# Optimization experiments

Hardware: AMD Instinct MI355X
Metric: run time of the kernel (lower is better)

Reference implementation:

```python
import math
import jax, jax.numpy as jnp
import numpy as np

B, T = 65536, 34
VOCAB, TOK_DIM, POS_DIM, D_MODEL, FFN_DIM, HEAD_DIM = 14, 2, 3, 5, 2, 5
EPS = 1e-5

def _pos_flat_idx():
    # replicate _build_pos_map: 10 digits, Z_HI, 10 digits, Z_HI, 10 digits, special0, special1
    sources, indices = [], []
    for _ in range(3):
        for i in range(10):
            sources.append(0); indices.append(i)
        sources.append(2); indices.append(len([s for s in sources if s == 2]) - 1)
    # fix: the torch code appends (2,0),(2,1) after first two digit blocks and (1,0),(2,2) after the third
    sources, indices = [], []
    for i in range(10): sources.append(0); indices.append(i)
    sources.append(2); indices.append(0)
    for i in range(10): sources.append(0); indices.append(i)
    sources.append(2); indices.append(1)
    for i in range(10): sources.append(0); indices.append(i)
    sources.append(1); indices.append(0)
    sources.append(2); indices.append(2)
    src = np.array(sources); idx = np.array(indices)
    # table layout: rows 0..9 digit_pos, row 10 z_hi_pos, rows 11..13 special (learned0, learned1, eos)
    offs = np.array([0, 10, 11])
    return offs[src] + idx  # (34,)

POS_FLAT = jnp.asarray(_pos_flat_idx())
CAUSAL = jnp.tril(jnp.ones((T, T), dtype=bool))

def _rms(x, w):
    return x * jax.lax.rsqrt(jnp.mean(x * x, -1, keepdims=True) + EPS) * w

def setup_inputs():
    key = jax.random.key(0)
    ks = jax.random.split(key, 16)
    n = lambda i, shape: jax.random.normal(ks[i], shape, jnp.float32) * 0.5
    return {
        'idx': jax.random.randint(ks[0], (B, T), 0, VOCAB),
        'tok_emb': n(1, (VOCAB, TOK_DIM)),
        'spiral_amp': jnp.float32(1.0),
        'spiral_phase': jnp.float32(0.1),
        'spiral_slope': jnp.float32(1.0 / 9.0),
        'spiral_offset': jnp.float32(0.05),
        'pos_corr_slope': jnp.float32(0.01),
        'pos_corr_intercept': jnp.float32(0.02),
        'z_hi_pos': n(2, (1, POS_DIM)),
        'special_pos': n(3, (2, POS_DIM)),
        'q_w': n(4, (HEAD_DIM, POS_DIM)),
        'v_w': n(5, (HEAD_DIM, TOK_DIM)),
        'out_A': n(6, (HEAD_DIM, 2)),
        'out_B': n(7, (2, D_MODEL)),
        'q_phase': n(8, (1,)),
        'ln1_w': jnp.ones((D_MODEL,), jnp.float32),
        'ln2_w': jnp.ones((D_MODEL,), jnp.float32),
        'lnf_w': jnp.ones((D_MODEL,), jnp.float32),
        'fc1_w': n(9, (FFN_DIM, D_MODEL)),
        'fc1_b': n(10, (FFN_DIM,)),
        'fc2_w': n(11, (D_MODEL, FFN_DIM)),
        'fc2_b': n(12, (D_MODEL,)),
        'head_w': n(13, (TOK_DIM, D_MODEL)),
    }

def reference(idx, tok_emb, spiral_amp, spiral_phase, spiral_slope, spiral_offset,
              pos_corr_slope, pos_corr_intercept, z_hi_pos, special_pos,
              q_w, v_w, out_A, out_B, q_phase, ln1_w, ln2_w, lnf_w,
              fc1_w, fc1_b, fc2_w, fc2_b, head_w):
    # learned spiral digit positions (10, 3)
    i = jnp.arange(10, dtype=jnp.float32)
    angle = 2.0 * math.pi * i / 10.0 + spiral_phase
    base = jnp.stack([spiral_amp * jnp.cos(angle),
                      spiral_amp * jnp.sin(angle),
                      spiral_slope * i + spiral_offset], -1)
    corr = pos_corr_intercept + pos_corr_slope * i
    digit_pos = base * (1.0 + corr)[:, None]
    table = jnp.concatenate([digit_pos, z_hi_pos, special_pos,
                             jnp.zeros((1, POS_DIM), jnp.float32)], 0)  # (14, 3)
    pos = table[POS_FLAT]  # (T, 3)

    tok = tok_emb[idx]  # (B, T, 2)
    x = jnp.concatenate([tok, jnp.broadcast_to(pos, (idx.shape[0], T, POS_DIM))], -1)  # (B,T,5)

    h = _rms(x, ln1_w)
    q = jnp.einsum('btp,dp->btd', h[..., TOK_DIM:], q_w)  # (B,T,5)
    k = q  # q_proj applied to same input for both q and k
    v = jnp.einsum('btp,dp->btd', h[..., :TOK_DIM], v_w)  # (B,T,5)

    # per-head 2D rotation on first 4 dims (HEAD_DIM//2 = 2 pairs), dim 4 unchanged
    c, s = jnp.cos(q_phase[0]), jnp.sin(q_phase[0])
    q0, q1 = q[..., 0:4:2], q[..., 1:4:2]
    q_rot = jnp.concatenate([
        jnp.stack([q0 * c - q1 * s, q0 * s + q1 * c], -1).reshape(q.shape[:-1] + (4,)),
        q[..., 4:]], -1)

    att = jnp.einsum('btd,bsd->bts', q_rot, k) / math.sqrt(HEAD_DIM)
    att = jnp.where(CAUSAL, att, -jnp.inf)
    att = jax.nn.softmax(att, -1)
    out = jnp.einsum('bts,bsd->btd', att, v)  # (B,T,5)

    x = x + (out @ out_A) @ out_B  # low-rank out_proj
    hh = _rms(x, ln2_w)
    x = x + (jax.nn.gelu(hh @ fc1_w.T + fc1_b, approximate=False) @ fc2_w.T + fc2_b)
    x = _rms(x, lnf_w)
    return (x @ head_w.T) @ tok_emb.T  # (B, T, 14)
```

## Files before the change

kernel.cpp:

```cpp
#include <hip/hip_runtime.h>
#include <math.h>

#define T_SEQ 34
#define NTOK 14
#define NE (T_SEQ * NTOK)
#define ROWS 15
#define BLK 512
#define NEL (ROWS * T_SEQ)
#define TTS 17

__global__ __launch_bounds__(BLK) void micro_fused_kernel(
    const int* __restrict__ idx,
    const float* __restrict__ tok_emb,
    const float* __restrict__ s_amp, const float* __restrict__ s_phase,
    const float* __restrict__ s_slope, const float* __restrict__ s_offset,
    const float* __restrict__ pc_slope, const float* __restrict__ pc_int,
    const float* __restrict__ z_hi, const float* __restrict__ spec,
    const float* __restrict__ q_w, const float* __restrict__ v_w,
    const float* __restrict__ out_A, const float* __restrict__ out_B,
    const float* __restrict__ q_phase,
    const float* __restrict__ ln1_w, const float* __restrict__ ln2_w,
    const float* __restrict__ lnf_w,
    const float* __restrict__ fc1_w, const float* __restrict__ fc1_b,
    const float* __restrict__ fc2_w, const float* __restrict__ fc2_b,
    const float* __restrict__ head_w,
    float* __restrict__ out, int N)
{
    __shared__ float4 H4[NE];
    __shared__ float  H1f[NE];
    __shared__ float4 C3[NE];
    __shared__ int    toksT[T_SEQ * TTS];
    alignas(16) __shared__ float PosT[T_SEQ * 3];
    alignas(16) __shared__ float TE[NTOK * 2];
    alignas(16) __shared__ float PMs[12];
    alignas(16) __shared__ float WsT[NTOK * 8];
    alignas(16) __shared__ float ln2s[8], lnfs[8], fc1ws[12], fc2ws[12], fc2bs[8];
    __shared__ float fc1bs[2];

    const int tid = threadIdx.x;
    const int elemBase = blockIdx.x * NEL;

    if (tid < NEL) {
        int g = elemBase + tid;
        int v = (g < N) ? idx[g] : 0;
        int r = tid / T_SEQ, s = tid - r * T_SEQ;
        toksT[s * TTS + r] = v;
    }

    if (tid < NE) {
        const float amp = s_amp[0], ph = s_phase[0], slp = s_slope[0], off = s_offset[0];
        const float pcs = pc_slope[0], pci = pc_int[0];
        const float cph = cosf(q_phase[0]), sph = sinf(q_phase[0]);
        const float cscale = 0.44721359549995793f * 1.4426950408889634f;
        const int e = tid;
        const int t = e / NTOK, tk = e - t * NTOK;
        float px, py, pz;
        if (t == 33)      { px = 0.f;     py = 0.f;     pz = 0.f; }
        else if (t == 32) { px = z_hi[0]; py = z_hi[1]; pz = z_hi[2]; }
        else if (t == 10) { px = spec[0]; py = spec[1]; pz = spec[2]; }
        else if (t == 21) { px = spec[3]; py = spec[4]; pz = spec[5]; }
        else {
            int i = (t < 10) ? t : (t < 21 ? t - 11 : t - 22);
            float fi = (float)i;
            float ang = 0.62831853071795864769f * fi + ph;
            float mlt = 1.f + pci + pcs * fi;
            px = amp * cosf(ang) * mlt;
            py = amp * sinf(ang) * mlt;
            pz = (slp * fi + off) * mlt;
        }
        if (tk == 0) { PosT[t*3] = px; PosT[t*3+1] = py; PosT[t*3+2] = pz; }
        float x0 = tok_emb[tk * 2], x1 = tok_emb[tk * 2 + 1];
        float ssum = x0*x0 + x1*x1 + px*px + py*py + pz*pz;
        float rn = rsqrtf(ssum * 0.2f + 1e-5f);
        float h0 = x0 * rn * ln1_w[0], h1 = x1 * rn * ln1_w[1];
        float h2 = px * rn * ln1_w[2], h3 = py * rn * ln1_w[3], h4 = pz * rn * ln1_w[4];
        float q0 = q_w[0]  * h2 + q_w[1]  * h3 + q_w[2]  * h4;
        float q1 = q_w[3]  * h2 + q_w[4]  * h3 + q_w[5]  * h4;
        float q2 = q_w[6]  * h2 + q_w[7]  * h3 + q_w[8]  * h4;
        float q3 = q_w[9]  * h2 + q_w[10] * h3 + q_w[11] * h4;
        float q4 = q_w[12] * h2 + q_w[13] * h3 + q_w[14] * h4;
        float r0 = q0 * cph - q1 * sph, r1 = q0 * sph + q1 * cph;
        float r2c = q2 * cph - q3 * sph, r3 = q2 * sph + q3 * cph;
        float c0 = (r0*q_w[0] + r1*q_w[3] + r2c*q_w[6] + r3*q_w[9]  + q4*q_w[12]) * cscale;
        float c1 = (r0*q_w[1] + r1*q_w[4] + r2c*q_w[7] + r3*q_w[10] + q4*q_w[13]) * cscale;
        float c2 = (r0*q_w[2] + r1*q_w[5] + r2c*q_w[8] + r3*q_w[11] + q4*q_w[14]) * cscale;
        H4[e] = make_float4(h2, h3, h4, h0);
        H1f[e] = h1;
        C3[e] = make_float4(c0, c1, c2, 0.f);
    }
    if (tid < 28) TE[tid] = tok_emb[tid];
    if (tid < 70) {
        int v = tid / 5, d = tid - v * 5;
        WsT[v * 8 + d] = head_w[d] * tok_emb[v * 2] + head_w[5 + d] * tok_emb[v * 2 + 1];
    }
    if (tid < 10) {
        int j = tid >> 1, c = tid & 1;
        float acc = 0.f;
        for (int i = 0; i < 5; ++i) {
            float m5 = out_A[i*2] * out_B[j] + out_A[i*2+1] * out_B[5 + j];
            acc += m5 * v_w[i*2 + c];
        }
        PMs[tid] = acc;
    }
    if (tid < 5)  { ln2s[tid] = ln2_w[tid]; lnfs[tid] = lnf_w[tid]; fc2bs[tid] = fc2_b[tid]; }
    if (tid < 10) { fc1ws[tid] = fc1_w[tid]; fc2ws[tid] = fc2_w[tid]; }
    if (tid < 2)  { fc1bs[tid] = fc1_b[tid]; }

    __syncthreads();

    if (tid >= NEL) return;
    const int t = tid / ROWS;
    const int r = tid - t * ROWS;
    const int lin = elemBase + r * T_SEQ + t;

    const int tokt = toksT[t * TTS + r];
    const float4 c3 = C3[t * NTOK + tokt];
    float l = 0.f, a0 = 0.f, a1 = 0.f;
#pragma unroll 4
    for (int s = 0; s <= t; ++s) {
        int tok = toksT[s * TTS + r];
        int e = s * NTOK + tok;
        float4 h = H4[e];
        float h1v = H1f[e];
        float sc = fmaf(c3.x, h.x, fmaf(c3.y, h.y, c3.z * h.z));
        float p = __builtin_amdgcn_exp2f(sc);
        l += p;
        a0 = fmaf(p, h.w, a0);
        a1 = fmaf(p, h1v, a1);
    }
    const float il = __builtin_amdgcn_rcpf(l);
    a0 *= il; a1 *= il;

    if (lin >= N) return;

    const float xv0 = TE[tokt * 2], xv1 = TE[tokt * 2 + 1];
    const float xv2 = PosT[t*3], xv3 = PosT[t*3+1], xv4 = PosT[t*3+2];

    float y[5];
    y[0] = xv0 + PMs[0] * a0 + PMs[1] * a1;
    y[1] = xv1 + PMs[2] * a0 + PMs[3] * a1;
    y[2] = xv2 + PMs[4] * a0 + PMs[5] * a1;
    y[3] = xv3 + PMs[6] * a0 + PMs[7] * a1;
    y[4] = xv4 + PMs[8] * a0 + PMs[9] * a1;

    float s2 = y[0]*y[0] + y[1]*y[1] + y[2]*y[2] + y[3]*y[3] + y[4]*y[4];
    float r2 = rsqrtf(s2 * 0.2f + 1e-5f);
    float hh[5];
#pragma unroll
    for (int j = 0; j < 5; ++j) hh[j] = y[j] * r2 * ln2s[j];

    float u0 = fc1bs[0], u1 = fc1bs[1];
#pragma unroll
    for (int j = 0; j < 5; ++j) { u0 += hh[j] * fc1ws[j]; u1 += hh[j] * fc1ws[5 + j]; }
    float g0 = 0.5f * u0 * (1.f + erff(u0 * 0.70710678118654752f));
    float g1v = 0.5f * u1 * (1.f + erff(u1 * 0.70710678118654752f));

    float y2[5]; float s3 = 0.f;
#pragma unroll
    for (int j = 0; j < 5; ++j) {
        y2[j] = y[j] + g0 * fc2ws[j * 2] + g1v * fc2ws[j * 2 + 1] + fc2bs[j];
        s3 += y2[j] * y2[j];
    }
    float r3 = rsqrtf(s3 * 0.2f + 1e-5f);
    float z[5];
#pragma unroll
    for (int j = 0; j < 5; ++j) z[j] = y2[j] * r3 * lnfs[j];

    float2* op = (float2*)(out + (size_t)lin * 14);
#pragma unroll
    for (int v = 0; v < 7; ++v) {
        float4 w0 = *(const float4*)&WsT[(2*v) * 8];
        float  w4 = WsT[(2*v) * 8 + 4];
        float4 u0v = *(const float4*)&WsT[(2*v+1) * 8];
        float  u4 = WsT[(2*v+1) * 8 + 4];
        float rA = z[0]*w0.x + z[1]*w0.y + z[2]*w0.z + z[3]*w0.w + z[4]*w4;
        float rB = z[0]*u0v.x + z[1]*u0v.y + z[2]*u0v.z + z[3]*u0v.w + z[4]*u4;
        op[v] = make_float2(rA, rB);
    }
}

extern "C" void kernel_launch(void* const* d_in, const int* in_sizes, int n_in,
                              void* d_out, int out_size, void* d_ws, size_t ws_size,
                              hipStream_t stream) {
    const int N = in_sizes[0];
    const int grid = (N + NEL - 1) / NEL;
    micro_fused_kernel<<<grid, BLK, 0, stream>>>(
        (const int*)d_in[0],
        (const float*)d_in[1], (const float*)d_in[2], (const float*)d_in[3],
        (const float*)d_in[4], (const float*)d_in[5], (const float*)d_in[6],
        (const float*)d_in[7], (const float*)d_in[8], (const float*)d_in[9],
        (const float*)d_in[10], (const float*)d_in[11], (const float*)d_in[12],
        (const float*)d_in[13], (const float*)d_in[14], (const float*)d_in[15],
        (const float*)d_in[16], (const float*)d_in[17], (const float*)d_in[18],
        (const float*)d_in[19], (const float*)d_in[20], (const float*)d_in[21],
        (const float*)d_in[22],
        (float*)d_out, N);
}
```

Measured before the change: 214.4 us.

## Process two sequences per thread and fold final RMS weight into head

Each block now covers 30 sequences instead of 15, and each active thread runs the causal-attention loop for two sequences at once, sharing the per-position index math and giving two independent dependency chains. The final RMS-norm weight is folded into the precomputed head/embedding matrix so the epilogue only scales by the norm factor. This halves the number of blocks and amortises the per-block table setup, but only 510 of 512 threads stay active after setup and register use per thread rises.

```diff
diff --git a/kernel.cpp b/kernel.cpp
--- a/kernel.cpp
+++ b/kernel.cpp
@@ -4,10 +4,11 @@
 #define T_SEQ 34
 #define NTOK 14
 #define NE (T_SEQ * NTOK)
-#define ROWS 15
+#define ROWS 30
+#define HR 15
 #define BLK 512
 #define NEL (ROWS * T_SEQ)
-#define TTS 17
+#define TTS 31
 
 __global__ __launch_bounds__(BLK) void micro_fused_kernel(
     const int* __restrict__ idx,
@@ -33,17 +34,17 @@
     alignas(16) __shared__ float PosT[T_SEQ * 3];
     alignas(16) __shared__ float TE[NTOK * 2];
     alignas(16) __shared__ float PMs[12];
-    alignas(16) __shared__ float WsT[NTOK * 8];
-    alignas(16) __shared__ float ln2s[8], lnfs[8], fc1ws[12], fc2ws[12], fc2bs[8];
+    alignas(16) __shared__ float Ws2[NTOK * 8];
+    alignas(16) __shared__ float ln2s[8], fc1ws[12], fc2ws[12], fc2bs[8];
     __shared__ float fc1bs[2];
 
     const int tid = threadIdx.x;
     const int elemBase = blockIdx.x * NEL;
 
-    if (tid < NEL) {
-        int g = elemBase + tid;
+    for (int i = tid; i < NEL; i += BLK) {
+        int g = elemBase + i;
         int v = (g < N) ? idx[g] : 0;
-        int r = tid / T_SEQ, s = tid - r * T_SEQ;
+        int r = i / T_SEQ, s = i - r * T_SEQ;
         toksT[s * TTS + r] = v;
     }
 
@@ -91,7 +92,8 @@
     if (tid < 28) TE[tid] = tok_emb[tid];
     if (tid < 70) {
         int v = tid / 5, d = tid - v * 5;
-        WsT[v * 8 + d] = head_w[d] * tok_emb[v * 2] + head_w[5 + d] * tok_emb[v * 2 + 1];
+        Ws2[v * 8 + d] = lnf_w[d] * (head_w[d] * tok_emb[v * 2]
+                                   + head_w[5 + d] * tok_emb[v * 2 + 1]);
     }
     if (tid < 10) {
         int j = tid >> 1, c = tid & 1;
@@ -102,81 +104,91 @@
         }
         PMs[tid] = acc;
     }
-    if (tid < 5)  { ln2s[tid] = ln2_w[tid]; lnfs[tid] = lnf_w[tid]; fc2bs[tid] = fc2_b[tid]; }
+    if (tid < 5)  { ln2s[tid] = ln2_w[tid]; fc2bs[tid] = fc2_b[tid]; }
     if (tid < 10) { fc1ws[tid] = fc1_w[tid]; fc2ws[tid] = fc2_w[tid]; }
     if (tid < 2)  { fc1bs[tid] = fc1_b[tid]; }
 
     __syncthreads();
 
-    if (tid >= NEL) return;
-    const int t = tid / ROWS;
-    const int r = tid - t * ROWS;
-    const int lin = elemBase + r * T_SEQ + t;
-
-    const int tokt = toksT[t * TTS + r];
-    const float4 c3 = C3[t * NTOK + tokt];
-    float l = 0.f, a0 = 0.f, a1 = 0.f;
+    if (tid >= HR * T_SEQ) return;
+    const int t  = tid / HR;
+    const int rA = tid - t * HR;
+    const int rB = rA + HR;
+
+    const int tokA = toksT[t * TTS + rA];
+    const int tokB = toksT[t * TTS + rB];
+    const float4 cA = C3[t * NTOK + tokA];
+    const float4 cB = C3[t * NTOK + tokB];
+
+    float lA = 0.f, aA0 = 0.f, aA1 = 0.f;
+    float lB = 0.f, aB0 = 0.f, aB1 = 0.f;
 #pragma unroll 4
     for (int s = 0; s <= t; ++s) {
-        int tok = toksT[s * TTS + r];
-        int e = s * NTOK + tok;
-        float4 h = H4[e];
-        float h1v = H1f[e];
-        float sc = fmaf(c3.x, h.x, fmaf(c3.y, h.y, c3.z * h.z));
-        float p = __builtin_amdgcn_exp2f(sc);
-        l += p;
-        a0 = fmaf(p, h.w, a0);
-        a1 = fmaf(p, h1v, a1);
-    }
-    const float il = __builtin_amdgcn_rcpf(l);
-    a0 *= il; a1 *= il;
-
-    if (lin >= N) return;
-
-    const float xv0 = TE[tokt * 2], xv1 = TE[tokt * 2 + 1];
-    const float xv2 = PosT[t*3], xv3 = PosT[t*3+1], xv4 = PosT[t*3+2];
-
-    float y[5];
-    y[0] = xv0 + PMs[0] * a0 + PMs[1] * a1;
-    y[1] = xv1 + PMs[2] * a0 + PMs[3] * a1;
-    y[2] = xv2 + PMs[4] * a0 + PMs[5] * a1;
-    y[3] = xv3 + PMs[6] * a0 + PMs[7] * a1;
-    y[4] = xv4 + PMs[8] * a0 + PMs[9] * a1;
-
-    float s2 = y[0]*y[0] + y[1]*y[1] + y[2]*y[2] + y[3]*y[3] + y[4]*y[4];
-    float r2 = rsqrtf(s2 * 0.2f + 1e-5f);
-    float hh[5];
-#pragma unroll
-    for (int j = 0; j < 5; ++j) hh[j] = y[j] * r2 * ln2s[j];
-
-    float u0 = fc1bs[0], u1 = fc1bs[1];
-#pragma unroll
-    for (int j = 0; j < 5; ++j) { u0 += hh[j] * fc1ws[j]; u1 += hh[j] * fc1ws[5 + j]; }
-    float g0 = 0.5f * u0 * (1.f + erff(u0 * 0.70710678118654752f));
-    float g1v = 0.5f * u1 * (1.f + erff(u1 * 0.70710678118654752f));
-
-    float y2[5]; float s3 = 0.f;
-#pragma unroll
-    for (int j = 0; j < 5; ++j) {
-        y2[j] = y[j] + g0 * fc2ws[j * 2] + g1v * fc2ws[j * 2 + 1] + fc2bs[j];
-        s3 += y2[j] * y2[j];
-    }
-    float r3 = rsqrtf(s3 * 0.2f + 1e-5f);
-    float z[5];
-#pragma unroll
-    for (int j = 0; j < 5; ++j) z[j] = y2[j] * r3 * lnfs[j];
-
-    float2* op = (float2*)(out + (size_t)lin * 14);
-#pragma unroll
-    for (int v = 0; v < 7; ++v) {
-        float4 w0 = *(const float4*)&WsT[(2*v) * 8];
-        float  w4 = WsT[(2*v) * 8 + 4];
-        float4 u0v = *(const float4*)&WsT[(2*v+1) * 8];
-        float  u4 = WsT[(2*v+1) * 8 + 4];
-        float rA = z[0]*w0.x + z[1]*w0.y + z[2]*w0.z + z[3]*w0.w + z[4]*w4;
-        float rB = z[0]*u0v.x + z[1]*u0v.y + z[2]*u0v.z + z[3]*u0v.w + z[4]*u4;
-        op[v] = make_float2(rA, rB);
-    }
+        int ta = toksT[s * TTS + rA];
+        int tb = toksT[s * TTS + rB];
+        int eA = s * NTOK + ta;
+        int eB = s * NTOK + tb;
+        float4 hA = H4[eA]; float hA1 = H1f[eA];
+        float4 hB = H4[eB]; float hB1 = H1f[eB];
+        float scA = fmaf(cA.x, hA.x, fmaf(cA.y, hA.y, cA.z * hA.z));
+        float scB = fmaf(cB.x, hB.x, fmaf(cB.y, hB.y, cB.z * hB.z));
+        float pA = __builtin_amdgcn_exp2f(scA);
+        float pB = __builtin_amdgcn_exp2f(scB);
+        lA += pA; aA0 = fmaf(pA, hA.w, aA0); aA1 = fmaf(pA, hA1, aA1);
+        lB += pB; aB0 = fmaf(pB, hB.w, aB0); aB1 = fmaf(pB, hB1, aB1);
+    }
+    const float ilA = __builtin_amdgcn_rcpf(lA);
+    const float ilB = __builtin_amdgcn_rcpf(lB);
+    aA0 *= ilA; aA1 *= ilA;
+    aB0 *= ilB; aB1 *= ilB;
+
+    const float pxv = PosT[t*3], pyv = PosT[t*3+1], pzv = PosT[t*3+2];
+
+    auto epi = [&](int r, int tok, float a0, float a1) {
+        const int lin = elemBase + r * T_SEQ + t;
+        if (lin >= N) return;
+        float y[5];
+        y[0] = TE[tok*2]   + PMs[0] * a0 + PMs[1] * a1;
+        y[1] = TE[tok*2+1] + PMs[2] * a0 + PMs[3] * a1;
+        y[2] = pxv + PMs[4] * a0 + PMs[5] * a1;
+        y[3] = pyv + PMs[6] * a0 + PMs[7] * a1;
+        y[4] = pzv + PMs[8] * a0 + PMs[9] * a1;
+
+        float s2 = y[0]*y[0] + y[1]*y[1] + y[2]*y[2] + y[3]*y[3] + y[4]*y[4];
+        float r2 = rsqrtf(s2 * 0.2f + 1e-5f);
+        float hh[5];
+#pragma unroll
+        for (int j = 0; j < 5; ++j) hh[j] = y[j] * r2 * ln2s[j];
+
+        float u0 = fc1bs[0], u1 = fc1bs[1];
+#pragma unroll
+        for (int j = 0; j < 5; ++j) { u0 += hh[j] * fc1ws[j]; u1 += hh[j] * fc1ws[5 + j]; }
+        float g0 = 0.5f * u0 * (1.f + erff(u0 * 0.70710678118654752f));
+        float g1v = 0.5f * u1 * (1.f + erff(u1 * 0.70710678118654752f));
+
+        float y2[5]; float s3 = 0.f;
+#pragma unroll
+        for (int j = 0; j < 5; ++j) {
+            y2[j] = y[j] + g0 * fc2ws[j * 2] + g1v * fc2ws[j * 2 + 1] + fc2bs[j];
+            s3 += y2[j] * y2[j];
+        }
+        float r3 = rsqrtf(s3 * 0.2f + 1e-5f);
+
+        float2* op = (float2*)(out + (size_t)lin * 14);
+#pragma unroll
+        for (int v = 0; v < 7; ++v) {
+            float4 w0 = *(const float4*)&Ws2[(2*v) * 8];
+            float  w4 = Ws2[(2*v) * 8 + 4];
+            float4 u0v = *(const float4*)&Ws2[(2*v+1) * 8];
+            float  u4 = Ws2[(2*v+1) * 8 + 4];
+            float rAo = r3 * (y2[0]*w0.x + y2[1]*w0.y + y2[2]*w0.z + y2[3]*w0.w + y2[4]*w4);
+            float rBo = r3 * (y2[0]*u0v.x + y2[1]*u0v.y + y2[2]*u0v.z + y2[3]*u0v.w + y2[4]*u4);
+            op[v] = make_float2(rAo, rBo);
+        }
+    };
+
+    epi(rA, tokA, aA0, aA1);
+    epi(rB, tokB, aB0, aB1);
 }
 
 extern "C" void kernel_launch(void* const* d_in, const int* in_sizes, int n_in,
```

Result: no change. 214.9 us (+0.2%).
